# Optimization experiments

Measured on AMD Instinct MI355X. Metric: run time of the kernel, lower is better.

Reference implementation:

```python
import jax, jax.numpy as jnp
import numpy as np

N, D = 131072, 128   # total nodes, feature size (input_size)
G, L = 512, 448      # num graphs, max padded segment length
EPS = 1e-5


def setup_inputs() -> dict:
    key = jax.random.key(0)
    ks = jax.random.split(key, 8)
    # ragged segment sizes summing exactly to N, each <= L
    rng = np.random.default_rng(0)
    counts = rng.integers(192, 321, size=G)
    diff = N - int(counts.sum())
    idx = rng.integers(0, G, size=abs(diff))
    np.add.at(counts, idx, 1 if diff > 0 else -1)
    assert int(counts.sum()) == N and int(counts.max()) <= L
    batch = jnp.asarray(np.repeat(np.arange(G), counts), dtype=jnp.int32)

    s = 1.0 / np.sqrt(D)
    x = jax.random.normal(ks[0], (N, D), jnp.float32)
    Wk = jax.random.normal(ks[1], (D, D), jnp.float32) * s
    Wq = jax.random.normal(ks[2], (D, D), jnp.float32) * s
    Wv = jax.random.normal(ks[3], (D, D), jnp.float32) * s
    bk = jnp.zeros((D,), jnp.float32)
    bq = jnp.zeros((D,), jnp.float32)
    bv = jnp.zeros((D,), jnp.float32)
    gamma = jnp.ones((D,), jnp.float32)
    beta = jnp.zeros((D,), jnp.float32)
    return {"x": x, "Wk": Wk, "bk": bk, "Wq": Wq, "bq": bq,
            "Wv": Wv, "bv": bv, "gamma": gamma, "beta": beta, "batch": batch}


def reference(x, Wk, bk, Wq, bq, Wv, bv, gamma, beta, batch):
    keys = x @ Wk.T + bk
    query = x @ Wq.T + bq
    values = x @ Wv.T + bv

    counts = jnp.bincount(batch, length=G)                 # [G]
    starts = jnp.cumsum(counts) - counts                   # segment offsets
    pos = jnp.arange(N, dtype=batch.dtype) - starts[batch]  # index within segment

    # scatter ragged nodes into padded [G, L, D] blocks (honors block-diagonal structure)
    kp = jnp.zeros((G, L, D), x.dtype).at[batch, pos].set(keys)
    qp = jnp.zeros((G, L, D), x.dtype).at[batch, pos].set(query)
    vp = jnp.zeros((G, L, D), x.dtype).at[batch, pos].set(values)
    valid = jnp.arange(L)[None, :] < counts[:, None]        # [G, L]

    # NOTE: original computes softmax(K @ Q^T / sqrt(dk)) @ V (keys as rows)
    scale = 1.0 / jnp.sqrt(jnp.asarray(D, x.dtype))
    scores = jnp.einsum('gld,gmd->glm', kp, qp) * scale     # [G, L, L]
    scores = jnp.where(valid[:, None, :], scores, jnp.asarray(-1e9, x.dtype))
    attn = jax.nn.softmax(scores, axis=-1)
    zp = jnp.einsum('glm,gmd->gld', attn, vp)               # [G, L, D]
    z = zp[batch, pos]                                      # back to ragged [N, D]

    h = x + z
    mu = jnp.mean(h, axis=-1, keepdims=True)
    var = jnp.var(h, axis=-1, keepdims=True)
    return (h - mu) / jnp.sqrt(var + EPS) * gamma + beta
```

## Files before the change

### kernel.cpp

```cpp
#include <hip/hip_runtime.h>
#include <hip/hip_bf16.h>

#define N_NODES 131072
#define DIM 128
#define NG 512

typedef __bf16 bf16;
typedef __attribute__((ext_vector_type(8))) __bf16 bf16x8;
typedef __attribute__((ext_vector_type(4))) float f32x4;

#define WS_STARTS 0
#define WS_WB     8192
#define WS_KB     131072
#define WS_QB     (131072 + 33554432)
#define WS_VTB    (131072 + 2*33554432)

__global__ void seg_starts_kernel(const int* __restrict__ batch, int* __restrict__ starts) {
    int g = threadIdx.x;
    int lo = 0, hi = N_NODES;
    while (lo < hi) { int mid = (lo + hi) >> 1; if (batch[mid] < g) lo = mid + 1; else hi = mid; }
    starts[g] = lo;
    if (g == 0) starts[NG] = N_NODES;
}

__global__ void wconv_kernel(const float* __restrict__ Wk, const float* __restrict__ Wq,
                             const float* __restrict__ Wv, bf16* __restrict__ Wb) {
    int e = blockIdx.x * 256 + threadIdx.x;
    int mat = e >> 14, idx = e & 16383;
    const float* src = (mat == 0) ? Wk : ((mat == 1) ? Wq : Wv);
    Wb[e] = (bf16)src[idx];
}

__global__ __launch_bounds__(256) void qkv_kernel(
        const float* __restrict__ x, const bf16* __restrict__ Wb,
        const float* __restrict__ bk, const float* __restrict__ bq, const float* __restrict__ bv,
        bf16* __restrict__ Kb, bf16* __restrict__ Qb, bf16* __restrict__ Vtb) {
    __shared__ bf16 vt[128 * 136];
    const int tid = threadIdx.x;
    const int w = tid >> 6, lane = tid & 63, q = lane >> 4, i = lane & 15;
    const int r0 = blockIdx.x * 128;

    bf16x8 af[2][4];
    for (int rg = 0; rg < 2; rg++) {
        const float* xr = x + (size_t)(r0 + w * 32 + rg * 16 + i) * DIM;
        for (int ks = 0; ks < 4; ks++) {
            const float4* p = (const float4*)(xr + ks * 32 + q * 8);
            float4 u0 = p[0], u1 = p[1];
            bf16x8 v;
            v[0]=(bf16)u0.x; v[1]=(bf16)u0.y; v[2]=(bf16)u0.z; v[3]=(bf16)u0.w;
            v[4]=(bf16)u1.x; v[5]=(bf16)u1.y; v[6]=(bf16)u1.z; v[7]=(bf16)u1.w;
            af[rg][ks] = v;
        }
    }
    for (int mat = 0; mat < 3; mat++) {
        const bf16* Wm = Wb + mat * (DIM * DIM);
        const float* bias = (mat == 0) ? bk : ((mat == 1) ? bq : bv);
        bf16* outp = (mat == 0) ? Kb : ((mat == 1) ? Qb : (bf16*)0);
        for (int n0 = 0; n0 < 8; n0++) {
            int col = n0 * 16 + i;
            float bias_v = bias[col];
            f32x4 acc0 = {0,0,0,0}, acc1 = {0,0,0,0};
            for (int ks = 0; ks < 4; ks++) {
                bf16x8 bw = *(const bf16x8*)(Wm + col * DIM + ks * 32 + q * 8);
                acc0 = __builtin_amdgcn_mfma_f32_16x16x32_bf16(af[0][ks], bw, acc0, 0, 0, 0);
                acc1 = __builtin_amdgcn_mfma_f32_16x16x32_bf16(af[1][ks], bw, acc1, 0, 0, 0);
            }
            for (int rg = 0; rg < 2; rg++) {
                f32x4 a = rg ? acc1 : acc0;
                for (int r = 0; r < 4; r++) {
                    int rowl = w * 32 + rg * 16 + q * 4 + r;
                    bf16 hv = (bf16)(a[r] + bias_v);
                    if (mat < 2) outp[(size_t)(r0 + rowl) * DIM + col] = hv;
                    else         vt[col * 136 + rowl] = hv;
                }
            }
        }
    }
    __syncthreads();
    {
        int d = tid >> 1, half = tid & 1;
        const uint4* src = (const uint4*)(vt + d * 136 + half * 64);
        uint4* dst = (uint4*)(Vtb + (size_t)d * N_NODES + r0 + half * 64);
        #pragma unroll
        for (int j = 0; j < 8; j++) dst[j] = src[j];
    }
}

__global__ __launch_bounds__(256) void attn_kernel(
        const float* __restrict__ x,
        const bf16* __restrict__ Kb, const bf16* __restrict__ Qb, const bf16* __restrict__ Vtb,
        const float* __restrict__ gamma, const float* __restrict__ beta,
        const int* __restrict__ starts, float* __restrict__ out) {
    __shared__ bf16 Ks[64 * 136];
    __shared__ bf16 Qs[64 * 136];
    __shared__ bf16 Vts[128 * 72];
    __shared__ bf16 Ps[4 * 16 * 72];

    const int g = blockIdx.y;
    const int seg = starts[g];
    const int c = starts[g + 1] - seg;
    const int l0 = blockIdx.x * 64;
    if (l0 >= c) return;

    const int tid = threadIdx.x;
    const int w = tid >> 6, lane = tid & 63, q = lane >> 4, i = lane & 15;

    {
        int row = tid >> 4;
        int col8 = (tid & 15) * 8;
        for (int p = 0; p < 4; p++, row += 16) {
            uint4 v = {0,0,0,0};
            int l = l0 + row;
            if (l < c) v = *(const uint4*)(Kb + (size_t)(seg + l) * DIM + col8);
            *(uint4*)&Ks[row * 136 + col8] = v;
        }
    }
    __syncthreads();

    bf16x8 afK[4];
    #pragma unroll
    for (int ks = 0; ks < 4; ks++)
        afK[ks] = *(const bf16x8*)&Ks[(w * 16 + i) * 136 + ks * 32 + q * 8];

    float mi[4], li[4];
    f32x4 Oc[8];
    #pragma unroll
    for (int r = 0; r < 4; r++) { mi[r] = -3.0e38f; li[r] = 0.0f; }
    #pragma unroll
    for (int t = 0; t < 8; t++) Oc[t] = (f32x4){0,0,0,0};

    const float kSc = 0.08838834764831845f * 1.4426950408889634f;

    const int cid0 = seg >> 6, cid1 = (seg + c - 1) >> 6;
    for (int cid = cid0; cid <= cid1; cid++) {
        const int a = cid << 6;
        __syncthreads();
        {
            int row = tid >> 4;
            int col8 = (tid & 15) * 8;
            for (int p = 0; p < 4; p++, row += 16) {
                uint4 v = *(const uint4*)(Qb + (size_t)(a + row) * DIM + col8);
                *(uint4*)&Qs[row * 136 + col8] = v;
            }
        }
        {
            int d = tid >> 3;
            int m8 = (tid & 7) * 8;
            for (int p = 0; p < 4; p++, d += 32) {
                uint4 v = *(const uint4*)(Vtb + (size_t)d * N_NODES + a + m8);
                *(uint4*)&Vts[d * 72 + m8] = v;
            }
        }
        __syncthreads();

        f32x4 s[4];
        #pragma unroll
        for (int ti = 0; ti < 4; ti++) {
            f32x4 acc = {0,0,0,0};
            #pragma unroll
            for (int ks = 0; ks < 4; ks++) {
                bf16x8 bq = *(const bf16x8*)&Qs[(ti * 16 + i) * 136 + ks * 32 + q * 8];
                acc = __builtin_amdgcn_mfma_f32_16x16x32_bf16(afK[ks], bq, acc, 0, 0, 0);
            }
            s[ti] = acc;
        }
        float m4[4] = {-3.0e38f, -3.0e38f, -3.0e38f, -3.0e38f};
        #pragma unroll
        for (int ti = 0; ti < 4; ti++) {
            int mg = a + ti * 16 + i;
            bool valid = (mg >= seg) && (mg < seg + c);
            #pragma unroll
            for (int r = 0; r < 4; r++) {
                float sv = valid ? s[ti][r] * kSc : -1.0e30f;
                s[ti][r] = sv;
                m4[r] = fmaxf(m4[r], sv);
            }
        }
        #pragma unroll
        for (int st = 1; st < 16; st <<= 1)
            #pragma unroll
            for (int r = 0; r < 4; r++)
                m4[r] = fmaxf(m4[r], __shfl_xor(m4[r], st));
        float alpha[4], rs[4];
        #pragma unroll
        for (int r = 0; r < 4; r++) {
            float mn = fmaxf(mi[r], m4[r]);
            alpha[r] = exp2f(mi[r] - mn);
            mi[r] = mn;
            rs[r] = 0.0f;
        }
        #pragma unroll
        for (int ti = 0; ti < 4; ti++)
            #pragma unroll
            for (int r = 0; r < 4; r++) {
                float pv = exp2f(s[ti][r] - mi[r]);
                s[ti][r] = pv;
                rs[r] += pv;
            }
        #pragma unroll
        for (int st = 1; st < 16; st <<= 1)
            #pragma unroll
            for (int r = 0; r < 4; r++)
                rs[r] += __shfl_xor(rs[r], st);
        #pragma unroll
        for (int r = 0; r < 4; r++) li[r] = li[r] * alpha[r] + rs[r];
        #pragma unroll
        for (int t = 0; t < 8; t++)
            #pragma unroll
            for (int r = 0; r < 4; r++)
                Oc[t][r] *= alpha[r];

        bf16* Pw = Ps + w * (16 * 72);
        #pragma unroll
        for (int ti = 0; ti < 4; ti++)
            #pragma unroll
            for (int r = 0; r < 4; r++)
                Pw[(q * 4 + r) * 72 + ti * 16 + i] = (bf16)s[ti][r];

        bf16x8 afP[2];
        #pragma unroll
        for (int k2 = 0; k2 < 2; k2++)
            afP[k2] = *(const bf16x8*)&Pw[i * 72 + k2 * 32 + q * 8];
        #pragma unroll
        for (int dt = 0; dt < 8; dt++) {
            #pragma unroll
            for (int k2 = 0; k2 < 2; k2++) {
                bf16x8 bv = *(const bf16x8*)&Vts[(dt * 16 + i) * 72 + k2 * 32 + q * 8];
                Oc[dt] = __builtin_amdgcn_mfma_f32_16x16x32_bf16(afP[k2], bv, Oc[dt], 0, 0, 0);
            }
        }
    }

    float gv[8], bvv[8];
    #pragma unroll
    for (int ti = 0; ti < 8; ti++) { gv[ti] = gamma[ti * 16 + i]; bvv[ti] = beta[ti * 16 + i]; }
    for (int r = 0; r < 4; r++) {
        int lg = l0 + w * 16 + q * 4 + r;
        if (lg >= c) continue;
        size_t node = (size_t)(seg + lg);
        float inv = 1.0f / li[r];
        const float* xr = x + node * DIM;
        float h[8], sum = 0.0f, ss = 0.0f;
        #pragma unroll
        for (int ti = 0; ti < 8; ti++) {
            float hv = xr[ti * 16 + i] + Oc[ti][r] * inv;
            h[ti] = hv;
            sum += hv; ss += hv * hv;
        }
        #pragma unroll
        for (int st = 1; st < 16; st <<= 1) {
            sum += __shfl_xor(sum, st);
            ss  += __shfl_xor(ss, st);
        }
        float mu = sum * (1.0f / 128.0f);
        float var = ss * (1.0f / 128.0f) - mu * mu;
        float rstd = rsqrtf(var + 1e-5f);
        float* op = out + node * DIM;
        #pragma unroll
        for (int ti = 0; ti < 8; ti++)
            op[ti * 16 + i] = (h[ti] - mu) * rstd * gv[ti] + bvv[ti];
    }
}

extern "C" void kernel_launch(void* const* d_in, const int* in_sizes, int n_in,
                              void* d_out, int out_size, void* d_ws, size_t ws_size,
                              hipStream_t stream) {
    (void)in_sizes; (void)n_in; (void)out_size; (void)ws_size;
    const float* x     = (const float*)d_in[0];
    const float* Wk    = (const float*)d_in[1];
    const float* bk    = (const float*)d_in[2];
    const float* Wq    = (const float*)d_in[3];
    const float* bq    = (const float*)d_in[4];
    const float* Wv    = (const float*)d_in[5];
    const float* bv    = (const float*)d_in[6];
    const float* gamma = (const float*)d_in[7];
    const float* beta  = (const float*)d_in[8];
    const int*   batch = (const int*)d_in[9];
    float* out = (float*)d_out;

    char* ws = (char*)d_ws;
    int*  starts = (int*)(ws + WS_STARTS);
    bf16* Wb  = (bf16*)(ws + WS_WB);
    bf16* Kb  = (bf16*)(ws + WS_KB);
    bf16* Qb  = (bf16*)(ws + WS_QB);
    bf16* Vtb = (bf16*)(ws + WS_VTB);

    seg_starts_kernel<<<1, 512, 0, stream>>>(batch, starts);
    wconv_kernel<<<192, 256, 0, stream>>>(Wk, Wq, Wv, Wb);
    qkv_kernel<<<1024, 256, 0, stream>>>(x, Wb, bk, bq, bv, Kb, Qb, Vtb);
    attn_kernel<<<dim3(7, NG), 256, 0, stream>>>(x, Kb, Qb, Vtb, gamma, beta, starts, out);
}
```

Measured before the change: 302.2 us.

## Stage K/Q stores through LDS and read K/Q fragments directly from global

In the QKV projection, K and Q outputs are now staged through the shared tile and written back as coalesced 16-byte row stores, like V already was, instead of scattered 2-byte global stores. In the attention kernel, the LDS staging buffers for K and Q are removed. Each wave now loads its MFMA fragments straight from global memory, clamping out-of-range rows. This cuts LDS usage and block syncs, which may raise occupancy, but every wave now re-reads Q tiles from global/L2 instead of sharing one LDS copy per block.

Result: slower. 371.1 us (+22.8%).

```diff
diff --git a/kernel.cpp b/kernel.cpp
--- a/kernel.cpp
+++ b/kernel.cpp
@@ -35,7 +35,7 @@
         const float* __restrict__ x, const bf16* __restrict__ Wb,
         const float* __restrict__ bk, const float* __restrict__ bq, const float* __restrict__ bv,
         bf16* __restrict__ Kb, bf16* __restrict__ Qb, bf16* __restrict__ Vtb) {
-    __shared__ bf16 vt[128 * 136];
+    __shared__ bf16 tile[128 * 136];
     const int tid = threadIdx.x;
     const int w = tid >> 6, lane = tid & 63, q = lane >> 4, i = lane & 15;
     const int r0 = blockIdx.x * 128;
@@ -55,7 +55,6 @@
     for (int mat = 0; mat < 3; mat++) {
         const bf16* Wm = Wb + mat * (DIM * DIM);
         const float* bias = (mat == 0) ? bk : ((mat == 1) ? bq : bv);
-        bf16* outp = (mat == 0) ? Kb : ((mat == 1) ? Qb : (bf16*)0);
         for (int n0 = 0; n0 < 8; n0++) {
             int col = n0 * 16 + i;
             float bias_v = bias[col];
@@ -70,19 +69,23 @@
                 for (int r = 0; r < 4; r++) {
                     int rowl = w * 32 + rg * 16 + q * 4 + r;
                     bf16 hv = (bf16)(a[r] + bias_v);
-                    if (mat < 2) outp[(size_t)(r0 + rowl) * DIM + col] = hv;
-                    else         vt[col * 136 + rowl] = hv;
+                    if (mat < 2) tile[rowl * 136 + col] = hv;
+                    else         tile[col * 136 + rowl] = hv;
                 }
             }
         }
-    }
-    __syncthreads();
-    {
-        int d = tid >> 1, half = tid & 1;
-        const uint4* src = (const uint4*)(vt + d * 136 + half * 64);
-        uint4* dst = (uint4*)(Vtb + (size_t)d * N_NODES + r0 + half * 64);
-        #pragma unroll
-        for (int j = 0; j < 8; j++) dst[j] = src[j];
+        __syncthreads();
+        {
+            int row = tid >> 1, half = tid & 1;
+            const uint4* src = (const uint4*)(tile + row * 136 + half * 64);
+            uint4* dst;
+            if (mat == 0)      dst = (uint4*)(Kb  + (size_t)(r0 + row) * DIM + half * 64);
+            else if (mat == 1) dst = (uint4*)(Qb  + (size_t)(r0 + row) * DIM + half * 64);
+            else               dst = (uint4*)(Vtb + (size_t)row * N_NODES + r0 + half * 64);
+            #pragma unroll
+            for (int j = 0; j < 8; j++) dst[j] = src[j];
+        }
+        __syncthreads();
     }
 }
 
@@ -91,8 +94,6 @@
         const bf16* __restrict__ Kb, const bf16* __restrict__ Qb, const bf16* __restrict__ Vtb,
         const float* __restrict__ gamma, const float* __restrict__ beta,
         const int* __restrict__ starts, float* __restrict__ out) {
-    __shared__ bf16 Ks[64 * 136];
-    __shared__ bf16 Qs[64 * 136];
     __shared__ bf16 Vts[128 * 72];
     __shared__ bf16 Ps[4 * 16 * 72];
 
@@ -105,22 +106,15 @@
     const int tid = threadIdx.x;
     const int w = tid >> 6, lane = tid & 63, q = lane >> 4, i = lane & 15;
 
+    bf16x8 afK[4];
     {
-        int row = tid >> 4;
-        int col8 = (tid & 15) * 8;
-        for (int p = 0; p < 4; p++, row += 16) {
-            uint4 v = {0,0,0,0};
-            int l = l0 + row;
-            if (l < c) v = *(const uint4*)(Kb + (size_t)(seg + l) * DIM + col8);
-            *(uint4*)&Ks[row * 136 + col8] = v;
-        }
-    }
-    __syncthreads();
-
-    bf16x8 afK[4];
-    #pragma unroll
-    for (int ks = 0; ks < 4; ks++)
-        afK[ks] = *(const bf16x8*)&Ks[(w * 16 + i) * 136 + ks * 32 + q * 8];
+        int lrow = l0 + w * 16 + i;
+        if (lrow > c - 1) lrow = c - 1;
+        const bf16* krow = Kb + (size_t)(seg + lrow) * DIM;
+        #pragma unroll
+        for (int ks = 0; ks < 4; ks++)
+            afK[ks] = *(const bf16x8*)(krow + ks * 32 + q * 8);
+    }
 
     float mi[4], li[4];
     f32x4 Oc[8];
@@ -136,14 +130,6 @@
         const int a = cid << 6;
         __syncthreads();
         {
-            int row = tid >> 4;
-            int col8 = (tid & 15) * 8;
-            for (int p = 0; p < 4; p++, row += 16) {
-                uint4 v = *(const uint4*)(Qb + (size_t)(a + row) * DIM + col8);
-                *(uint4*)&Qs[row * 136 + col8] = v;
-            }
-        }
-        {
             int d = tid >> 3;
             int m8 = (tid & 7) * 8;
             for (int p = 0; p < 4; p++, d += 32) {
@@ -159,7 +145,7 @@
             f32x4 acc = {0,0,0,0};
             #pragma unroll
             for (int ks = 0; ks < 4; ks++) {
-                bf16x8 bq = *(const bf16x8*)&Qs[(ti * 16 + i) * 136 + ks * 32 + q * 8];
+                bf16x8 bq = *(const bf16x8*)(Qb + (size_t)(a + ti * 16 + i) * DIM + ks * 32 + q * 8);
                 acc = __builtin_amdgcn_mfma_f32_16x16x32_bf16(afK[ks], bq, acc, 0, 0, 0);
             }
             s[ti] = acc;
```
